# Performance work log

Hardware: AMD Instinct MI355X
Metric: run time of the kernel (lower is better)

Reference implementation:

```python
import jax, jax.numpy as jnp
import numpy as np

V, D, H, C = 50000, 300, 128, 10  # vocab, embed_dim, hidden_size, num_classes
B, T = 128, 512


def _lstm_dir(x, w_ih, w_hh, b_ih, b_hh, reverse):
    # x: [B,T,Din]; w_ih: [4H,Din]; w_hh: [4H,H]; biases: [4H]
    xg = jnp.einsum('btd,gd->btg', x, w_ih) + b_ih + b_hh  # [B,T,4H]
    h0 = jnp.zeros((x.shape[0], H), x.dtype)

    def step(carry, xg_t):
        h, c = carry
        gates = xg_t + h @ w_hh.T
        i, f, g, o = jnp.split(gates, 4, axis=-1)  # PyTorch gate order i,f,g,o
        i = jax.nn.sigmoid(i); f = jax.nn.sigmoid(f)
        g = jnp.tanh(g); o = jax.nn.sigmoid(o)
        c = f * c + i * g
        h = o * jnp.tanh(c)
        return (h, c), h

    _, hs = jax.lax.scan(step, (h0, h0), jnp.swapaxes(xg, 0, 1), reverse=reverse)
    return jnp.swapaxes(hs, 0, 1)  # [B,T,H], aligned to input time order


def _bilstm_layer(x, wf, wr):
    hf = _lstm_dir(x, *wf, reverse=False)
    hr = _lstm_dir(x, *wr, reverse=True)
    return jnp.concatenate([hf, hr], axis=-1)  # [B,T,2H]


def setup_inputs() -> dict:
    key = jax.random.key(0)
    ks = iter(jax.random.split(key, 24))
    inp = {"x": jax.random.randint(next(ks), (B, T), 0, V, dtype=jnp.int64).astype(jnp.int32)}
    inp["emb"] = jax.random.normal(next(ks), (V, D), jnp.float32) * 0.1
    s = 1.0 / np.sqrt(H)
    def lw(din, k1, k2, k3, k4):
        return (jax.random.uniform(k1, (4 * H, din), jnp.float32, -s, s),
                jax.random.uniform(k2, (4 * H, H), jnp.float32, -s, s),
                jax.random.uniform(k3, (4 * H,), jnp.float32, -s, s),
                jax.random.uniform(k4, (4 * H,), jnp.float32, -s, s))
    for name, din in [("l0f", D), ("l0r", D), ("l1f", 2 * H), ("l1r", 2 * H)]:
        w_ih, w_hh, b_ih, b_hh = lw(din, next(ks), next(ks), next(ks), next(ks))
        inp[f"w_ih_{name}"] = w_ih
        inp[f"w_hh_{name}"] = w_hh
        inp[f"b_ih_{name}"] = b_ih
        inp[f"b_hh_{name}"] = b_hh
    inp["fc_w"] = jax.random.normal(next(ks), (C, 2 * H), jnp.float32) * 0.05
    inp["fc_b"] = jnp.zeros((C,), jnp.float32)
    return inp


def reference(x, emb,
              w_ih_l0f, w_hh_l0f, b_ih_l0f, b_hh_l0f,
              w_ih_l0r, w_hh_l0r, b_ih_l0r, b_hh_l0r,
              w_ih_l1f, w_hh_l1f, b_ih_l1f, b_hh_l1f,
              w_ih_l1r, w_hh_l1r, b_ih_l1r, b_hh_l1r,
              fc_w, fc_b):
    h = emb[x]  # [B,T,D] embedding lookup
    h = _bilstm_layer(h, (w_ih_l0f, w_hh_l0f, b_ih_l0f, b_hh_l0f),
                      (w_ih_l0r, w_hh_l0r, b_ih_l0r, b_hh_l0r))
    h = _bilstm_layer(h, (w_ih_l1f, w_hh_l1f, b_ih_l1f, b_hh_l1f),
                      (w_ih_l1r, w_hh_l1r, b_ih_l1r, b_hh_l1r))
    return h[:, -1, :] @ fc_w.T + fc_b  # [B,C]
```

## Files before the change

### kernel.cpp

```cpp
#include <hip/hip_runtime.h>
#include <cstdint>
#include <cstddef>

#define T_SEQ 512
#define BATCH 128
#define HID   128
#define G4    512
#define NCLS  10

typedef unsigned short u16;
typedef unsigned int   u32;
typedef short bf16x8 __attribute__((ext_vector_type(8)));
typedef float f32x4  __attribute__((ext_vector_type(4)));

__device__ __forceinline__ float sigmoidf_(float x) {
    return 1.f / (1.f + __expf(-x));
}
__device__ __forceinline__ float tanhf_(float x) {
    return 2.f / (1.f + __expf(-2.f * x)) - 1.f;
}

__device__ __forceinline__ u16 bf16rne(float f) {
    u32 u = __float_as_uint(f);
    u32 r = (u + 0x7fffu + ((u >> 16) & 1u)) >> 16;
    return (u16)r;
}
__device__ __forceinline__ float bf16tof(u16 s) {
    return __uint_as_float(((u32)s) << 16);
}
__device__ __forceinline__ uint4 pack8(const u16* h) {
    uint4 u;
    u.x = (u32)h[0] | ((u32)h[1] << 16);
    u.y = (u32)h[2] | ((u32)h[3] << 16);
    u.z = (u32)h[4] | ((u32)h[5] << 16);
    u.w = (u32)h[6] | ((u32)h[7] << 16);
    return u;
}

__global__ __launch_bounds__(256)
void prep_w(const float* __restrict__ w0f, const float* __restrict__ w0r,
            const float* __restrict__ w1f,
            u16* __restrict__ W0f1, u16* __restrict__ W0f2,
            u16* __restrict__ W0r1, u16* __restrict__ W0r2,
            u16* __restrict__ W1f1, u16* __restrict__ W1f2)
{
    int idx = blockIdx.x * 256 + threadIdx.x;
    if (idx < 512 * 320) {
        int r = idx / 320, k = idx - r * 320;
        float v = (k < 300) ? w0f[r * 300 + k] : 0.f;
        u16 a = bf16rne(v);
        W0f1[idx] = a; W0f2[idx] = bf16rne(v - bf16tof(a));
        v = (k < 300) ? w0r[r * 300 + k] : 0.f;
        a = bf16rne(v);
        W0r1[idx] = a; W0r2[idx] = bf16rne(v - bf16tof(a));
    }
    if (idx < 512 * 256) {
        float v = w1f[idx];
        u16 a = bf16rne(v);
        W1f1[idx] = a; W1f2[idx] = bf16rne(v - bf16tof(a));
    }
}

__global__ __launch_bounds__(256)
void gemm_mfma(const float* __restrict__ A, const int* __restrict__ rows,
               int lda, int Kp,
               const u16* __restrict__ W1, const u16* __restrict__ W2,
               const float* __restrict__ bih, const float* __restrict__ bhh,
               float* __restrict__ out, int tcshift, int tc0)
{
    __shared__ __align__(16) u16 lA1[128][40];
    __shared__ __align__(16) u16 lA2[128][40];
    __shared__ __align__(16) u16 lW1[128][40];
    __shared__ __align__(16) u16 lW2[128][40];

    const int tid = threadIdx.x;
    const int tn = blockIdx.x & 3;
    const int tm = blockIdx.x >> 2;
    const int m0 = tm * 128, n0 = tn * 128;

    const int wave = tid >> 6, lane = tid & 63;
    const int wm = wave & 1, wn = wave >> 1;
    const int quad = lane >> 4, l16 = lane & 15;

    const int srow = tid >> 1;
    const int sk   = (tid & 1) * 16;

    const float* arow;
    {
        int m  = m0 + srow;
        int b  = m >> tcshift;
        int tt = m & ((1 << tcshift) - 1);
        int grow = b * T_SEQ + tc0 + tt;
        int r = rows ? rows[grow] : grow;
        arow = A + (size_t)r * lda;
    }
    const u16* w1row = W1 + (size_t)(n0 + srow) * Kp + sk;
    const u16* w2row = W2 + (size_t)(n0 + srow) * Kp + sk;

    f32x4 acc[4][4];
#pragma unroll
    for (int i = 0; i < 4; i++)
#pragma unroll
        for (int j = 0; j < 4; j++) acc[i][j] = f32x4{0.f, 0.f, 0.f, 0.f};

    for (int k0 = 0; k0 < Kp; k0 += 32) {
        float av[16];
#pragma unroll
        for (int v = 0; v < 4; v++) {
            int k = k0 + sk + v * 4;
            float4 t = {0.f, 0.f, 0.f, 0.f};
            if (k + 4 <= lda) t = *(const float4*)(arow + k);
            av[v * 4 + 0] = t.x; av[v * 4 + 1] = t.y;
            av[v * 4 + 2] = t.z; av[v * 4 + 3] = t.w;
        }
        uint4 wv1a = *(const uint4*)(w1row + k0);
        uint4 wv1b = *(const uint4*)(w1row + k0 + 8);
        uint4 wv2a = *(const uint4*)(w2row + k0);
        uint4 wv2b = *(const uint4*)(w2row + k0 + 8);

        u16 h1[16], h2[16];
#pragma unroll
        for (int j = 0; j < 16; j++) {
            u16 a = bf16rne(av[j]);
            h1[j] = a;
            h2[j] = bf16rne(av[j] - bf16tof(a));
        }

        __syncthreads();
        *(uint4*)&lA1[srow][sk]     = pack8(h1);
        *(uint4*)&lA1[srow][sk + 8] = pack8(h1 + 8);
        *(uint4*)&lA2[srow][sk]     = pack8(h2);
        *(uint4*)&lA2[srow][sk + 8] = pack8(h2 + 8);
        *(uint4*)&lW1[srow][sk]     = wv1a;
        *(uint4*)&lW1[srow][sk + 8] = wv1b;
        *(uint4*)&lW2[srow][sk]     = wv2a;
        *(uint4*)&lW2[srow][sk + 8] = wv2b;
        __syncthreads();

        bf16x8 fa1[4], fa2[4], fw1[4], fw2[4];
#pragma unroll
        for (int t = 0; t < 4; t++) {
            int ar = wm * 64 + t * 16 + l16;
            int wr = wn * 64 + t * 16 + l16;
            fa1[t] = *(const bf16x8*)&lA1[ar][quad * 8];
            fa2[t] = *(const bf16x8*)&lA2[ar][quad * 8];
            fw1[t] = *(const bf16x8*)&lW1[wr][quad * 8];
            fw2[t] = *(const bf16x8*)&lW2[wr][quad * 8];
        }

#pragma unroll
        for (int mt = 0; mt < 4; mt++)
#pragma unroll
            for (int nt = 0; nt < 4; nt++)
                acc[mt][nt] = __builtin_amdgcn_mfma_f32_16x16x32_bf16(
                    fa1[mt], fw1[nt], acc[mt][nt], 0, 0, 0);
#pragma unroll
        for (int mt = 0; mt < 4; mt++)
#pragma unroll
            for (int nt = 0; nt < 4; nt++)
                acc[mt][nt] = __builtin_amdgcn_mfma_f32_16x16x32_bf16(
                    fa1[mt], fw2[nt], acc[mt][nt], 0, 0, 0);
#pragma unroll
        for (int mt = 0; mt < 4; mt++)
#pragma unroll
            for (int nt = 0; nt < 4; nt++)
                acc[mt][nt] = __builtin_amdgcn_mfma_f32_16x16x32_bf16(
                    fa2[mt], fw1[nt], acc[mt][nt], 0, 0, 0);
    }

#pragma unroll
    for (int nt = 0; nt < 4; nt++) {
        int n = n0 + wn * 64 + nt * 16 + l16;
        float bv = bih[n] + bhh[n];
#pragma unroll
        for (int mt = 0; mt < 4; mt++) {
            int mb = m0 + wm * 64 + mt * 16 + quad * 4;
#pragma unroll
            for (int r = 0; r < 4; r++)
                out[(size_t)(mb + r) * G4 + n] = acc[mt][nt][r] + bv;
        }
    }
}

template <int MODE>
__global__ __launch_bounds__(512, 2)
void lstm_rec(const float* __restrict__ xg0, const float* __restrict__ xg1,
              const float* __restrict__ whh_f, const float* __restrict__ whh_r,
              float* __restrict__ hout,
              float* __restrict__ hst_f, float* __restrict__ cst_f,
              float* __restrict__ hst_r, float* __restrict__ cst_r,
              int Tc, int tc0f, int tc0r, int first)
{
    const int wg  = blockIdx.x;
    const int dir = (MODE == 0) ? (wg >> 7) : 0;
    const int b   = wg & 127;
    const float* xgb = (dir ? xg1 : xg0) + (size_t)b * Tc * G4;
    const float* whh = dir ? whh_r : whh_f;
    float* hst = dir ? hst_r : hst_f;
    float* cst = dir ? cst_r : cst_f;
    const int tc0 = dir ? tc0r : tc0f;

    const int j = threadIdx.x;
    const int u = j >> 2;
    const int g = j & 3;
    const int row = g * HID + u;

    float w[128];
    {
        const float* wr = whh + (size_t)row * HID;
#pragma unroll
        for (int k = 0; k < 128; k += 4) {
            float4 t = *(const float4*)(wr + k);
            w[k] = t.x; w[k + 1] = t.y; w[k + 2] = t.z; w[k + 3] = t.w;
        }
    }

    __shared__ __align__(16) float h_s[2][HID];
    float c_rep = 0.f;
    if (j < HID) h_s[0][j] = first ? 0.f : hst[(size_t)b * HID + j];
    if (!first) c_rep = cst[(size_t)b * HID + u];
    __syncthreads();

    const float mg = (g == 2) ? 2.f : 1.f;

    int buf = 0;
    float xv = xgb[(size_t)(dir ? Tc - 1 : 0) * G4 + row];
    float hlast = 0.f;

    for (int s = 0; s < Tc; s++) {
        const int tt = dir ? (Tc - 1 - s) : s;
        float nxv = 0.f;
        if (s + 1 < Tc) {
            int ttn = dir ? (tt - 1) : (tt + 1);
            nxv = xgb[(size_t)ttn * G4 + row];
        }

        const float* hb = h_s[buf];
        float a0 = 0.f, a1 = 0.f, a2 = 0.f, a3 = 0.f;
#pragma unroll
        for (int k4 = 0; k4 < 32; k4++) {
            float4 h4 = *(const float4*)(hb + k4 * 4);
            int k = k4 * 4;
            a0 += w[k]     * h4.x;
            a1 += w[k + 1] * h4.y;
            a2 += w[k + 2] * h4.z;
            a3 += w[k + 3] * h4.w;
        }
        float a = xv + (a0 + a1) + (a2 + a3);

        float e = __expf(-mg * a);
        float v = mg / (1.f + e) - (mg - 1.f);

        float vi = __shfl(v, 0, 4);
        float vf = __shfl(v, 1, 4);
        float vg = __shfl(v, 2, 4);
        float vo = __shfl(v, 3, 4);

        c_rep = vf * c_rep + vi * vg;
        float th = 2.f / (1.f + __expf(-2.f * c_rep)) - 1.f;
        float hv = vo * th;
        hlast = hv;

        if (g == 0) {
            h_s[buf ^ 1][u] = hv;
            if (MODE == 0)
                hout[((size_t)b * T_SEQ + (tc0 + tt)) * 256 + dir * HID + u] = hv;
        }
        __syncthreads();
        buf ^= 1;
        xv = nxv;
    }

    if (g == 0) {
        hst[(size_t)b * HID + u] = hlast;
        cst[(size_t)b * HID + u] = c_rep;
    }
}

__global__ __launch_bounds__(512)
void final_k(const float* __restrict__ h0cat,
             const float* __restrict__ w_ih_r,
             const float* __restrict__ bih_r, const float* __restrict__ bhh_r,
             const float* __restrict__ h1f_last,
             const float* __restrict__ fc_w,
             const float* __restrict__ fc_b,
             float* __restrict__ out)
{
    int b = blockIdx.x;
    int j = threadIdx.x;
    __shared__ __align__(16) float hin[256];
    __shared__ __align__(16) float g_s[G4];
    __shared__ __align__(16) float hcat[256];

    if (j < 256) hin[j] = h0cat[((size_t)b * T_SEQ + (T_SEQ - 1)) * 256 + j];
    __syncthreads();

    float acc = bih_r[j] + bhh_r[j];
    const float* wr = w_ih_r + (size_t)j * 256;
#pragma unroll 8
    for (int k = 0; k < 256; k += 4) {
        float4 h4 = *(const float4*)&hin[k];
        float4 w4 = *(const float4*)&wr[k];
        acc += w4.x * h4.x + w4.y * h4.y + w4.z * h4.z + w4.w * h4.w;
    }
    float v = (j >= 256 && j < 384) ? tanhf_(acc) : sigmoidf_(acc);
    g_s[j] = v;
    if (j < 128) hcat[j] = h1f_last[(size_t)b * HID + j];
    __syncthreads();

    if (j < 128) {
        float gi = g_s[j], gg = g_s[j + 256], go = g_s[j + 384];
        float c = gi * gg;
        hcat[128 + j] = go * tanhf_(c);
    }
    __syncthreads();

    if (j < NCLS) {
        float a = fc_b[j];
        const float* fw = fc_w + (size_t)j * 256;
        for (int k = 0; k < 256; k++) a += fw[k] * hcat[k];
        out[(size_t)b * NCLS + j] = a;
    }
}

extern "C" void kernel_launch(void* const* d_in, const int* in_sizes, int n_in,
                              void* d_out, int out_size, void* d_ws, size_t ws_size,
                              hipStream_t stream)
{
    (void)in_sizes; (void)n_in; (void)out_size;

    const int*   x       = (const int*)  d_in[0];
    const float* emb     = (const float*)d_in[1];
    const float* wih_l0f = (const float*)d_in[2];
    const float* whh_l0f = (const float*)d_in[3];
    const float* bih_l0f = (const float*)d_in[4];
    const float* bhh_l0f = (const float*)d_in[5];
    const float* wih_l0r = (const float*)d_in[6];
    const float* whh_l0r = (const float*)d_in[7];
    const float* bih_l0r = (const float*)d_in[8];
    const float* bhh_l0r = (const float*)d_in[9];
    const float* wih_l1f = (const float*)d_in[10];
    const float* whh_l1f = (const float*)d_in[11];
    const float* bih_l1f = (const float*)d_in[12];
    const float* bhh_l1f = (const float*)d_in[13];
    const float* wih_l1r = (const float*)d_in[14];
    const float* whh_l1r = (const float*)d_in[15];
    const float* bih_l1r = (const float*)d_in[16];
    const float* bhh_l1r = (const float*)d_in[17];
    const float* fc_w    = (const float*)d_in[18];
    const float* fc_b    = (const float*)d_in[19];
    float* out = (float*)d_out;
    (void)whh_l1r;

    char* ws = (char*)d_ws;
    float* h0cat = (float*)ws;
    float* st    = (float*)(ws + (size_t)67108864);
    float* hst0 = st + 0 * 16384;
    float* cst0 = st + 1 * 16384;
    float* hst1 = st + 2 * 16384;
    float* cst1 = st + 3 * 16384;
    float* hst2 = st + 4 * 16384;
    float* cst2 = st + 5 * 16384;

    u16* wsp = (u16*)(ws + (size_t)67108864 + 393216);
    u16* W0f1 = wsp;
    u16* W0f2 = wsp + 163840;
    u16* W0r1 = wsp + 327680;
    u16* W0r2 = wsp + 491520;
    u16* W1f1 = wsp + 655360;
    u16* W1f2 = wsp + 786432;

    const size_t base = (size_t)67108864 + 393216 + 1835008;

    int Tc = 256;
    while (Tc > 32 && base + 2 * (size_t)262144 * Tc > ws_size) Tc >>= 1;
    const int NC = T_SEQ / Tc;
    int tcshift = 0;
    while ((1 << tcshift) < Tc) tcshift++;
    float* xgc0 = (float*)(ws + base);
    float* xgc1 = xgc0 + (size_t)BATCH * Tc * G4;

    const dim3 gemm_grid(Tc * 4);

    prep_w<<<dim3(640), 256, 0, stream>>>(
        wih_l0f, wih_l0r, wih_l1f, W0f1, W0f2, W0r1, W0r2, W1f1, W1f2);

    for (int i = 0; i < NC; i++) {
        int cf = i, cr = NC - 1 - i;
        gemm_mfma<<<gemm_grid, 256, 0, stream>>>(
            emb, x, 300, 320, W0f1, W0f2, bih_l0f, bhh_l0f,
            xgc0, tcshift, cf * Tc);
        gemm_mfma<<<gemm_grid, 256, 0, stream>>>(
            emb, x, 300, 320, W0r1, W0r2, bih_l0r, bhh_l0r,
            xgc1, tcshift, cr * Tc);
        lstm_rec<0><<<dim3(2 * BATCH), 512, 0, stream>>>(
            xgc0, xgc1, whh_l0f, whh_l0r, h0cat,
            hst0, cst0, hst1, cst1, Tc, cf * Tc, cr * Tc, i == 0);
    }

    for (int i = 0; i < NC; i++) {
        gemm_mfma<<<gemm_grid, 256, 0, stream>>>(
            h0cat, nullptr, 256, 256, W1f1, W1f2, bih_l1f, bhh_l1f,
            xgc0, tcshift, i * Tc);
        lstm_rec<1><<<dim3(BATCH), 512, 0, stream>>>(
            xgc0, nullptr, whh_l1f, nullptr, nullptr,
            hst2, cst2, nullptr, nullptr, Tc, i * Tc, 0, i == 0);
    }

    final_k<<<dim3(BATCH), 512, 0, stream>>>(
        h0cat, wih_l1r, bih_l1r, bhh_l1r, hst2, fc_w, fc_b, out);
}
```

Before: 1.397 ms.

## Split LSTM recurrent dot products across 8 lanes with shuffle reduction

The recurrent kernel moves from 512 threads each holding a full 128-wide weight row to 1024 threads per block. Each thread holds 16-wide slices of all four gate rows for one hidden unit, and the partial sums are combined with a butterfly transpose-reduce over xor shuffles. This shortens the serial per-step dot-product chain and cuts per-thread registers, which matters because each timestep is latency-bound. In exchange it adds shuffle rounds and a barrier over a larger block on every step, and it drops the 2-blocks-per-CU launch bound.

Result: slower. 1.466 ms (+5.0%).

```diff
diff --git a/kernel.cpp b/kernel.cpp
--- a/kernel.cpp
+++ b/kernel.cpp
@@ -183,7 +183,7 @@
 }
 
 template <int MODE>
-__global__ __launch_bounds__(512, 2)
+__global__ __launch_bounds__(1024)
 void lstm_rec(const float* __restrict__ xg0, const float* __restrict__ xg1,
               const float* __restrict__ whh_f, const float* __restrict__ whh_r,
               float* __restrict__ hout,
@@ -200,18 +200,21 @@
     float* cst = dir ? cst_r : cst_f;
     const int tc0 = dir ? tc0r : tc0f;
 
-    const int j = threadIdx.x;
-    const int u = j >> 2;
-    const int g = j & 3;
-    const int row = g * HID + u;
-
-    float w[128];
-    {
-        const float* wr = whh + (size_t)row * HID;
-#pragma unroll
-        for (int k = 0; k < 128; k += 4) {
-            float4 t = *(const float4*)(wr + k);
-            w[k] = t.x; w[k + 1] = t.y; w[k + 2] = t.z; w[k + 3] = t.w;
+    const int j  = threadIdx.x;
+    const int u  = j >> 3;
+    const int kq = j & 7;
+    const int gf = kq & 3;
+    const int row = gf * HID + u;
+
+    float w[4][16];
+#pragma unroll
+    for (int gi = 0; gi < 4; gi++) {
+        const float* wr = whh + (size_t)(gi * HID + u) * HID + kq * 16;
+#pragma unroll
+        for (int k4 = 0; k4 < 4; k4++) {
+            float4 t = *(const float4*)(wr + k4 * 4);
+            w[gi][k4 * 4 + 0] = t.x; w[gi][k4 * 4 + 1] = t.y;
+            w[gi][k4 * 4 + 2] = t.z; w[gi][k4 * 4 + 3] = t.w;
         }
     }
 
@@ -221,7 +224,7 @@
     if (!first) c_rep = cst[(size_t)b * HID + u];
     __syncthreads();
 
-    const float mg = (g == 2) ? 2.f : 1.f;
+    const float mg = (gf == 2) ? 2.f : 1.f;
 
     int buf = 0;
     float xv = xgb[(size_t)(dir ? Tc - 1 : 0) * G4 + row];
@@ -235,33 +238,48 @@
             nxv = xgb[(size_t)ttn * G4 + row];
         }
 
-        const float* hb = h_s[buf];
-        float a0 = 0.f, a1 = 0.f, a2 = 0.f, a3 = 0.f;
-#pragma unroll
-        for (int k4 = 0; k4 < 32; k4++) {
+        const float* hb = &h_s[buf][kq * 16];
+        float p0 = 0.f, p1 = 0.f, p2 = 0.f, p3 = 0.f;
+#pragma unroll
+        for (int k4 = 0; k4 < 4; k4++) {
             float4 h4 = *(const float4*)(hb + k4 * 4);
             int k = k4 * 4;
-            a0 += w[k]     * h4.x;
-            a1 += w[k + 1] * h4.y;
-            a2 += w[k + 2] * h4.z;
-            a3 += w[k + 3] * h4.w;
-        }
-        float a = xv + (a0 + a1) + (a2 + a3);
-
-        float e = __expf(-mg * a);
-        float v = mg / (1.f + e) - (mg - 1.f);
-
-        float vi = __shfl(v, 0, 4);
-        float vf = __shfl(v, 1, 4);
-        float vg = __shfl(v, 2, 4);
-        float vo = __shfl(v, 3, 4);
+            p0 += w[0][k] * h4.x; p1 += w[1][k] * h4.x; p2 += w[2][k] * h4.x; p3 += w[3][k] * h4.x;
+            p0 += w[0][k+1] * h4.y; p1 += w[1][k+1] * h4.y; p2 += w[2][k+1] * h4.y; p3 += w[3][k+1] * h4.y;
+            p0 += w[0][k+2] * h4.z; p1 += w[1][k+2] * h4.z; p2 += w[2][k+2] * h4.z; p3 += w[3][k+2] * h4.z;
+            p0 += w[0][k+3] * h4.w; p1 += w[1][k+3] * h4.w; p2 += w[2][k+3] * h4.w; p3 += w[3][k+3] * h4.w;
+        }
+
+        p0 += __shfl_xor(p0, 4, 64);
+        p1 += __shfl_xor(p1, 4, 64);
+        p2 += __shfl_xor(p2, 4, 64);
+        p3 += __shfl_xor(p3, 4, 64);
+        float s0 = (kq & 2) ? p0 : p2;
+        float s1 = (kq & 2) ? p1 : p3;
+        float r0 = __shfl_xor(s0, 2, 64);
+        float r1 = __shfl_xor(s1, 2, 64);
+        float q0 = ((kq & 2) ? p2 : p0) + r0;
+        float q1 = ((kq & 2) ? p3 : p1) + r1;
+        float s2 = (kq & 1) ? q0 : q1;
+        float r2 = __shfl_xor(s2, 1, 64);
+        float vv = ((kq & 1) ? q1 : q0) + r2;
+
+        vv += xv;
+
+        float e = __expf(-mg * vv);
+        float gv = mg / (1.f + e) - (mg - 1.f);
+
+        float vi = __shfl(gv, 0, 8);
+        float vf = __shfl(gv, 1, 8);
+        float vg = __shfl(gv, 2, 8);
+        float vo = __shfl(gv, 3, 8);
 
         c_rep = vf * c_rep + vi * vg;
         float th = 2.f / (1.f + __expf(-2.f * c_rep)) - 1.f;
         float hv = vo * th;
         hlast = hv;
 
-        if (g == 0) {
+        if (kq == 0) {
             h_s[buf ^ 1][u] = hv;
             if (MODE == 0)
                 hout[((size_t)b * T_SEQ + (tc0 + tt)) * 256 + dir * HID + u] = hv;
@@ -271,7 +289,7 @@
         xv = nxv;
     }
 
-    if (g == 0) {
+    if (kq == 0) {
         hst[(size_t)b * HID + u] = hlast;
         cst[(size_t)b * HID + u] = c_rep;
     }
@@ -393,7 +411,7 @@
         gemm_mfma<<<gemm_grid, 256, 0, stream>>>(
             emb, x, 300, 320, W0r1, W0r2, bih_l0r, bhh_l0r,
             xgc1, tcshift, cr * Tc);
-        lstm_rec<0><<<dim3(2 * BATCH), 512, 0, stream>>>(
+        lstm_rec<0><<<dim3(2 * BATCH), 1024, 0, stream>>>(
             xgc0, xgc1, whh_l0f, whh_l0r, h0cat,
             hst0, cst0, hst1, cst1, Tc, cf * Tc, cr * Tc, i == 0);
     }
@@ -402,7 +420,7 @@
         gemm_mfma<<<gemm_grid, 256, 0, stream>>>(
             h0cat, nullptr, 256, 256, W1f1, W1f2, bih_l1f, bhh_l1f,
             xgc0, tcshift, i * Tc);
-        lstm_rec<1><<<dim3(BATCH), 512, 0, stream>>>(
+        lstm_rec<1><<<dim3(BATCH), 1024, 0, stream>>>(
             xgc0, nullptr, whh_l1f, nullptr, nullptr,
             hst2, cst2, nullptr, nullptr, Tc, i * Tc, 0, i == 0);
     }
```

## Batch LSTM recurrence over 16 sequences per block using split-bf16 MFMA

Applied to the files above, without the earlier changes.

The recurrent h@W_hh step moves from per-sequence scalar FP32 dot products (one block per batch row) to 16-row batch tiles per block. Each tile computes the product with bf16 MFMA instructions, using a hi/lo split of both weights and hidden state to keep roughly FP32 accuracy. The recurrent weights are pre-split in the prep kernel and held in registers as MFMA fragments. The grid shrinks from 256/128 blocks to 16/8, so far fewer CUs are used. Each serial step now does more work per block, so latency depends on MFMA chain length and occupancy.

After: 2.758 ms. 1.97x slower.

```diff
diff --git a/kernel.cpp b/kernel.cpp
--- a/kernel.cpp
+++ b/kernel.cpp
@@ -40,9 +40,14 @@
 __global__ __launch_bounds__(256)
 void prep_w(const float* __restrict__ w0f, const float* __restrict__ w0r,
             const float* __restrict__ w1f,
+            const float* __restrict__ hh0f, const float* __restrict__ hh0r,
+            const float* __restrict__ hh1f,
             u16* __restrict__ W0f1, u16* __restrict__ W0f2,
             u16* __restrict__ W0r1, u16* __restrict__ W0r2,
-            u16* __restrict__ W1f1, u16* __restrict__ W1f2)
+            u16* __restrict__ W1f1, u16* __restrict__ W1f2,
+            u16* __restrict__ H0f1, u16* __restrict__ H0f2,
+            u16* __restrict__ H0r1, u16* __restrict__ H0r2,
+            u16* __restrict__ H1f1, u16* __restrict__ H1f2)
 {
     int idx = blockIdx.x * 256 + threadIdx.x;
     if (idx < 512 * 320) {
@@ -58,6 +63,17 @@
         float v = w1f[idx];
         u16 a = bf16rne(v);
         W1f1[idx] = a; W1f2[idx] = bf16rne(v - bf16tof(a));
+    }
+    if (idx < 512 * 128) {
+        float v = hh0f[idx];
+        u16 a = bf16rne(v);
+        H0f1[idx] = a; H0f2[idx] = bf16rne(v - bf16tof(a));
+        v = hh0r[idx];
+        a = bf16rne(v);
+        H0r1[idx] = a; H0r2[idx] = bf16rne(v - bf16tof(a));
+        v = hh1f[idx];
+        a = bf16rne(v);
+        H1f1[idx] = a; H1f2[idx] = bf16rne(v - bf16tof(a));
     }
 }
 
@@ -185,95 +201,140 @@
 template <int MODE>
 __global__ __launch_bounds__(512, 2)
 void lstm_rec(const float* __restrict__ xg0, const float* __restrict__ xg1,
-              const float* __restrict__ whh_f, const float* __restrict__ whh_r,
+              const u16* __restrict__ Wh1f, const u16* __restrict__ Wh2f,
+              const u16* __restrict__ Wh1r, const u16* __restrict__ Wh2r,
               float* __restrict__ hout,
               float* __restrict__ hst_f, float* __restrict__ cst_f,
               float* __restrict__ hst_r, float* __restrict__ cst_r,
               int Tc, int tc0f, int tc0r, int first)
 {
     const int wg  = blockIdx.x;
-    const int dir = (MODE == 0) ? (wg >> 7) : 0;
-    const int b   = wg & 127;
-    const float* xgb = (dir ? xg1 : xg0) + (size_t)b * Tc * G4;
-    const float* whh = dir ? whh_r : whh_f;
+    const int dir = (MODE == 0) ? (wg >> 3) : 0;
+    const int bt  = wg & 7;
+    const int b0  = bt * 16;
+    const float* xgb = dir ? xg1 : xg0;
+    const u16* Wh1 = dir ? Wh1r : Wh1f;
+    const u16* Wh2 = dir ? Wh2r : Wh2f;
     float* hst = dir ? hst_r : hst_f;
     float* cst = dir ? cst_r : cst_f;
     const int tc0 = dir ? tc0r : tc0f;
 
-    const int j = threadIdx.x;
-    const int u = j >> 2;
-    const int g = j & 3;
-    const int row = g * HID + u;
-
-    float w[128];
-    {
-        const float* wr = whh + (size_t)row * HID;
-#pragma unroll
-        for (int k = 0; k < 128; k += 4) {
-            float4 t = *(const float4*)(wr + k);
-            w[k] = t.x; w[k + 1] = t.y; w[k + 2] = t.z; w[k + 3] = t.w;
-        }
-    }
-
-    __shared__ __align__(16) float h_s[2][HID];
-    float c_rep = 0.f;
-    if (j < HID) h_s[0][j] = first ? 0.f : hst[(size_t)b * HID + j];
-    if (!first) c_rep = cst[(size_t)b * HID + u];
+    const int tid  = threadIdx.x;
+    const int wave = tid >> 6;
+    const int lane = tid & 63;
+    const int quad = lane >> 4;
+    const int l16  = lane & 15;
+    const int ut   = wave * 16 + l16;
+
+    bf16x8 fw1[4][4], fw2[4][4];
+#pragma unroll
+    for (int g = 0; g < 4; g++) {
+        const u16* p1 = Wh1 + (size_t)(g * 128 + ut) * 128 + quad * 8;
+        const u16* p2 = Wh2 + (size_t)(g * 128 + ut) * 128 + quad * 8;
+#pragma unroll
+        for (int kc = 0; kc < 4; kc++) {
+            fw1[g][kc] = *(const bf16x8*)(p1 + kc * 32);
+            fw2[g][kc] = *(const bf16x8*)(p2 + kc * 32);
+        }
+    }
+    asm volatile("" ::: "memory");
+
+    __shared__ u16 h1_s[2][16][136];
+    __shared__ u16 h2_s[2][16][136];
+
+#pragma unroll
+    for (int i = 0; i < 4; i++) {
+        int e = tid + 512 * i;
+        int m = e >> 7, u = e & 127;
+        float hv = first ? 0.f : hst[(size_t)(b0 + m) * HID + u];
+        u16 hi = bf16rne(hv);
+        h1_s[0][m][u] = hi;
+        h2_s[0][m][u] = bf16rne(hv - bf16tof(hi));
+    }
+    float c[4], hl[4];
+#pragma unroll
+    for (int r = 0; r < 4; r++) {
+        c[r]  = first ? 0.f : cst[(size_t)(b0 + quad * 4 + r) * HID + ut];
+        hl[r] = 0.f;
+    }
     __syncthreads();
 
-    const float mg = (g == 2) ? 2.f : 1.f;
+    const float* xp[4];
+#pragma unroll
+    for (int r = 0; r < 4; r++)
+        xp[r] = xgb + (size_t)(b0 + quad * 4 + r) * Tc * G4 + ut;
 
     int buf = 0;
-    float xv = xgb[(size_t)(dir ? Tc - 1 : 0) * G4 + row];
-    float hlast = 0.f;
-
     for (int s = 0; s < Tc; s++) {
         const int tt = dir ? (Tc - 1 - s) : s;
-        float nxv = 0.f;
-        if (s + 1 < Tc) {
-            int ttn = dir ? (tt - 1) : (tt + 1);
-            nxv = xgb[(size_t)ttn * G4 + row];
-        }
-
-        const float* hb = h_s[buf];
-        float a0 = 0.f, a1 = 0.f, a2 = 0.f, a3 = 0.f;
-#pragma unroll
-        for (int k4 = 0; k4 < 32; k4++) {
-            float4 h4 = *(const float4*)(hb + k4 * 4);
-            int k = k4 * 4;
-            a0 += w[k]     * h4.x;
-            a1 += w[k + 1] * h4.y;
-            a2 += w[k + 2] * h4.z;
-            a3 += w[k + 3] * h4.w;
-        }
-        float a = xv + (a0 + a1) + (a2 + a3);
-
-        float e = __expf(-mg * a);
-        float v = mg / (1.f + e) - (mg - 1.f);
-
-        float vi = __shfl(v, 0, 4);
-        float vf = __shfl(v, 1, 4);
-        float vg = __shfl(v, 2, 4);
-        float vo = __shfl(v, 3, 4);
-
-        c_rep = vf * c_rep + vi * vg;
-        float th = 2.f / (1.f + __expf(-2.f * c_rep)) - 1.f;
-        float hv = vo * th;
-        hlast = hv;
-
-        if (g == 0) {
-            h_s[buf ^ 1][u] = hv;
+
+        float xv[4][4];
+#pragma unroll
+        for (int g = 0; g < 4; g++)
+#pragma unroll
+            for (int r = 0; r < 4; r++)
+                xv[g][r] = xp[r][(size_t)tt * G4 + g * 128];
+
+        bf16x8 fa1[4], fa2[4];
+#pragma unroll
+        for (int kc = 0; kc < 4; kc++) {
+            fa1[kc] = *(const bf16x8*)&h1_s[buf][l16][kc * 32 + quad * 8];
+            fa2[kc] = *(const bf16x8*)&h2_s[buf][l16][kc * 32 + quad * 8];
+        }
+
+        f32x4 acc[4];
+#pragma unroll
+        for (int g = 0; g < 4; g++) acc[g] = f32x4{0.f, 0.f, 0.f, 0.f};
+
+#pragma unroll
+        for (int kc = 0; kc < 4; kc++)
+#pragma unroll
+            for (int g = 0; g < 4; g++)
+                acc[g] = __builtin_amdgcn_mfma_f32_16x16x32_bf16(
+                    fa1[kc], fw1[g][kc], acc[g], 0, 0, 0);
+#pragma unroll
+        for (int kc = 0; kc < 4; kc++)
+#pragma unroll
+            for (int g = 0; g < 4; g++)
+                acc[g] = __builtin_amdgcn_mfma_f32_16x16x32_bf16(
+                    fa1[kc], fw2[g][kc], acc[g], 0, 0, 0);
+#pragma unroll
+        for (int kc = 0; kc < 4; kc++)
+#pragma unroll
+            for (int g = 0; g < 4; g++)
+                acc[g] = __builtin_amdgcn_mfma_f32_16x16x32_bf16(
+                    fa2[kc], fw1[g][kc], acc[g], 0, 0, 0);
+
+#pragma unroll
+        for (int r = 0; r < 4; r++) {
+            float ai = acc[0][r] + xv[0][r];
+            float af = acc[1][r] + xv[1][r];
+            float ag = acc[2][r] + xv[2][r];
+            float ao = acc[3][r] + xv[3][r];
+            float vi = sigmoidf_(ai);
+            float vf = sigmoidf_(af);
+            float vg = tanhf_(ag);
+            float vo = sigmoidf_(ao);
+            c[r] = vf * c[r] + vi * vg;
+            float th = tanhf_(c[r]);
+            float hv = vo * th;
+            hl[r] = hv;
+            int m = quad * 4 + r;
+            u16 hi = bf16rne(hv);
+            h1_s[buf ^ 1][m][ut] = hi;
+            h2_s[buf ^ 1][m][ut] = bf16rne(hv - bf16tof(hi));
             if (MODE == 0)
-                hout[((size_t)b * T_SEQ + (tc0 + tt)) * 256 + dir * HID + u] = hv;
+                hout[((size_t)(b0 + m) * T_SEQ + (tc0 + tt)) * 256
+                     + dir * HID + ut] = hv;
         }
         __syncthreads();
         buf ^= 1;
-        xv = nxv;
-    }
-
-    if (g == 0) {
-        hst[(size_t)b * HID + u] = hlast;
-        cst[(size_t)b * HID + u] = c_rep;
+    }
+
+#pragma unroll
+    for (int r = 0; r < 4; r++) {
+        hst[(size_t)(b0 + quad * 4 + r) * HID + ut] = hl[r];
+        cst[(size_t)(b0 + quad * 4 + r) * HID + ut] = c[r];
     }
 }
 
@@ -369,8 +430,14 @@
     u16* W0r2 = wsp + 491520;
     u16* W1f1 = wsp + 655360;
     u16* W1f2 = wsp + 786432;
-
-    const size_t base = (size_t)67108864 + 393216 + 1835008;
+    u16* H0f1 = wsp + 917504;
+    u16* H0f2 = wsp + 983040;
+    u16* H0r1 = wsp + 1048576;
+    u16* H0r2 = wsp + 1114112;
+    u16* H1f1 = wsp + 1179648;
+    u16* H1f2 = wsp + 1245184;
+
+    const size_t base = (size_t)67108864 + 393216 + 2621440;
 
     int Tc = 256;
     while (Tc > 32 && base + 2 * (size_t)262144 * Tc > ws_size) Tc >>= 1;
@@ -383,7 +450,9 @@
     const dim3 gemm_grid(Tc * 4);
 
     prep_w<<<dim3(640), 256, 0, stream>>>(
-        wih_l0f, wih_l0r, wih_l1f, W0f1, W0f2, W0r1, W0r2, W1f1, W1f2);
+        wih_l0f, wih_l0r, wih_l1f, whh_l0f, whh_l0r, whh_l1f,
+        W0f1, W0f2, W0r1, W0r2, W1f1, W1f2,
+        H0f1, H0f2, H0r1, H0r2, H1f1, H1f2);
 
     for (int i = 0; i < NC; i++) {
         int cf = i, cr = NC - 1 - i;
@@ -393,8 +462,8 @@
         gemm_mfma<<<gemm_grid, 256, 0, stream>>>(
             emb, x, 300, 320, W0r1, W0r2, bih_l0r, bhh_l0r,
             xgc1, tcshift, cr * Tc);
-        lstm_rec<0><<<dim3(2 * BATCH), 512, 0, stream>>>(
-            xgc0, xgc1, whh_l0f, whh_l0r, h0cat,
+        lstm_rec<0><<<dim3(16), 512, 0, stream>>>(
+            xgc0, xgc1, H0f1, H0f2, H0r1, H0r2, h0cat,
             hst0, cst0, hst1, cst1, Tc, cf * Tc, cr * Tc, i == 0);
     }
 
@@ -402,8 +471,8 @@
         gemm_mfma<<<gemm_grid, 256, 0, stream>>>(
             h0cat, nullptr, 256, 256, W1f1, W1f2, bih_l1f, bhh_l1f,
             xgc0, tcshift, i * Tc);
-        lstm_rec<1><<<dim3(BATCH), 512, 0, stream>>>(
-            xgc0, nullptr, whh_l1f, nullptr, nullptr,
+        lstm_rec<1><<<dim3(8), 512, 0, stream>>>(
+            xgc0, nullptr, H1f1, H1f2, nullptr, nullptr, nullptr,
             hst2, cst2, nullptr, nullptr, Tc, i * Tc, 0, i == 0);
     }
 
```
